# Performance work log

Hardware: AMD Instinct MI355X
Metric: run time of the kernel (lower is better)

Reference implementation:

```python
import jax, jax.numpy as jnp
import numpy as np

B, S, D, H, DH, F = 4, 2048, 1024, 16, 64, 4096
EPS = 1e-5


def setup_inputs() -> dict:
    key = jax.random.key(0)
    ks = jax.random.split(key, 8)
    std = 0.02
    return {
        "src": jax.random.normal(ks[0], (B, S, D), dtype=jnp.float32),
        # per-head Q/K/V projections, stacked: [H, D, DH]
        "Wq": jax.random.normal(ks[1], (H, D, DH), dtype=jnp.float32) * std,
        "bq": jnp.zeros((H, DH), dtype=jnp.float32),
        "Wk": jax.random.normal(ks[2], (H, D, DH), dtype=jnp.float32) * std,
        "bk": jnp.zeros((H, DH), dtype=jnp.float32),
        "Wv": jax.random.normal(ks[3], (H, D, DH), dtype=jnp.float32) * std,
        "bv": jnp.zeros((H, DH), dtype=jnp.float32),
        "Wo": jax.random.normal(ks[4], (H * DH, D), dtype=jnp.float32) * std,
        "bo": jnp.zeros((D,), dtype=jnp.float32),
        "ln1_w": jnp.ones((D,), dtype=jnp.float32),
        "ln1_b": jnp.zeros((D,), dtype=jnp.float32),
        "W1": jax.random.normal(ks[5], (D, F), dtype=jnp.float32) * std,
        "b1": jnp.zeros((F,), dtype=jnp.float32),
        "W2": jax.random.normal(ks[6], (F, D), dtype=jnp.float32) * std,
        "b2": jnp.zeros((D,), dtype=jnp.float32),
        "ln2_w": jnp.ones((D,), dtype=jnp.float32),
        "ln2_b": jnp.zeros((D,), dtype=jnp.float32),
    }


def _layernorm(x, w, b):
    m = jnp.mean(x, axis=-1, keepdims=True)
    v = jnp.mean(jnp.square(x - m), axis=-1, keepdims=True)
    return (x - m) * jax.lax.rsqrt(v + EPS) * w + b


def reference(src, Wq, bq, Wk, bk, Wv, bv, Wo, bo, ln1_w, ln1_b, W1, b1, W2, b2, ln2_w, ln2_b):
    # Per-head projections, batched over heads: [B,H,S,DH]
    q = jnp.einsum('bsd,hde->bhse', src, Wq) + bq[None, :, None, :]
    k = jnp.einsum('bsd,hde->bhse', src, Wk) + bk[None, :, None, :]
    v = jnp.einsum('bsd,hde->bhse', src, Wv) + bv[None, :, None, :]
    scale = jnp.asarray(DH, src.dtype) ** 0.5
    scores = jnp.einsum('bhqe,bhke->bhqk', q, k) / scale  # [B,H,S,S]
    attn = jax.nn.softmax(scores, axis=-1)
    ctx = jnp.einsum('bhqk,bhke->bhqe', attn, v)  # [B,H,S,DH]
    # concat heads along feature dim (matches torch.cat over head outputs)
    ctx = ctx.transpose(0, 2, 1, 3).reshape(src.shape[0], src.shape[1], H * DH)
    attn_out = ctx @ Wo + bo
    x = _layernorm(src + attn_out, ln1_w, ln1_b)
    ffn = jax.nn.relu(x @ W1 + b1) @ W2 + b2
    return _layernorm(x + ffn, ln2_w, ln2_b)
```

## Files before the change

### kernel.cpp

```cpp
#include <hip/hip_runtime.h>
#include <stdint.h>


typedef unsigned short u16;
typedef __attribute__((ext_vector_type(8))) short short8;
typedef __attribute__((ext_vector_type(4))) float f32x4;
typedef __attribute__((ext_vector_type(16))) float f32x16;

__device__ __forceinline__ u16 f2bf(float f) {
  union { float f; unsigned u; } v; v.f = f;
  unsigned r = (v.u + 0x7fffu + ((v.u >> 16) & 1u)) >> 16;
  return (u16)r;
}

__device__ __forceinline__ void gl_lds16(const u16* g, u16* l) {
  __builtin_amdgcn_global_load_lds(
      (const __attribute__((address_space(1))) unsigned int*)g,
      (__attribute__((address_space(3))) unsigned int*)l, 16, 0, 0);
}

__device__ __forceinline__ unsigned cvtpk(float lo, float hi) {
  unsigned r;
  asm("v_cvt_pk_bf16_f32 %0, %1, %2" : "=v"(r) : "v"(lo), "v"(hi));
  return r;
}
__device__ __forceinline__ void pl32_swap(unsigned& a, unsigned& b) {
  asm("v_permlane32_swap_b32 %0, %1" : "+v"(a), "+v"(b));
}


__global__ __launch_bounds__(256) void transpose_cast(const float* __restrict__ W,
                                                      u16* __restrict__ WT,
                                                      int K, int N) {
  __shared__ u16 T[64 * 72];
  const int tid = threadIdx.x;
  const long n0 = (long)blockIdx.x * 64, k0 = (long)blockIdx.y * 64;
#pragma unroll
  for (int i = 0; i < 4; i++) {
    int c = tid + i * 256;
    int kr = c >> 4, nc = (c & 15) * 4;
    float4 v = *(const float4*)(W + (k0 + kr) * N + n0 + nc);
    T[(nc + 0) * 72 + kr] = f2bf(v.x);
    T[(nc + 1) * 72 + kr] = f2bf(v.y);
    T[(nc + 2) * 72 + kr] = f2bf(v.z);
    T[(nc + 3) * 72 + kr] = f2bf(v.w);
  }
  __syncthreads();
#pragma unroll
  for (int i = 0; i < 2; i++) {
    int c = tid + i * 256;
    int nr = c >> 3, kc = (c & 7) * 8;
    *(uint4*)(WT + (n0 + nr) * K + k0 + kc) = *(const uint4*)(T + nr * 72 + kc);
  }
}

__global__ __launch_bounds__(256) void transpose_cast_qkv(const float* __restrict__ Wq,
                                                          const float* __restrict__ Wk,
                                                          const float* __restrict__ Wv,
                                                          u16* __restrict__ WT) {
  __shared__ u16 T[64 * 72];
  const int tid = threadIdx.x;
  const int n0 = blockIdx.x * 64, k0 = blockIdx.y * 64;
  const float* W = (n0 < 1024) ? Wq : (n0 < 2048 ? Wk : Wv);
  const int h = (n0 & 1023) >> 6;
#pragma unroll
  for (int i = 0; i < 4; i++) {
    int c = tid + i * 256;
    int kr = c >> 4, ec = (c & 15) * 4;
    float4 v = *(const float4*)(W + ((long)h * 1024 + k0 + kr) * 64 + ec);
    T[(ec + 0) * 72 + kr] = f2bf(v.x);
    T[(ec + 1) * 72 + kr] = f2bf(v.y);
    T[(ec + 2) * 72 + kr] = f2bf(v.z);
    T[(ec + 3) * 72 + kr] = f2bf(v.w);
  }
  __syncthreads();
#pragma unroll
  for (int i = 0; i < 2; i++) {
    int c = tid + i * 256;
    int nr = c >> 3, kc = (c & 7) * 8;
    *(uint4*)(WT + ((long)(n0 + nr)) * 1024 + k0 + kc) = *(const uint4*)(T + nr * 72 + kc);
  }
}

__global__ __launch_bounds__(256) void cast_bf16(const float* __restrict__ x, u16* __restrict__ y) {
  const long i = ((long)blockIdx.x * 256 + threadIdx.x) * 8;
  float4 a = *(const float4*)(x + i);
  float4 b = *(const float4*)(x + i + 4);
  uint4 o;
  o.x = (unsigned)f2bf(a.x) | ((unsigned)f2bf(a.y) << 16);
  o.y = (unsigned)f2bf(a.z) | ((unsigned)f2bf(a.w) << 16);
  o.z = (unsigned)f2bf(b.x) | ((unsigned)f2bf(b.y) << 16);
  o.w = (unsigned)f2bf(b.z) | ((unsigned)f2bf(b.w) << 16);
  *(uint4*)(y + i) = o;
}

__global__ __launch_bounds__(256) void build_bcat(const float* __restrict__ bq,
                                                  const float* __restrict__ bk,
                                                  const float* __restrict__ bv,
                                                  float* __restrict__ bcat) {
  int i = blockIdx.x * 256 + threadIdx.x;
  const float* s = (i < 1024) ? bq : (i < 2048 ? bk : bv);
  bcat[i] = s[i & 1023];
}

#define GEMM_PROLOGUE                                                              \
  __shared__ __align__(16) u16 As[2][128 * 32];                                    \
  __shared__ __align__(16) u16 Bs[2][128 * 32];                                    \
  const int tid = threadIdx.x;                                                     \
  const int wave = tid >> 6, lane = tid & 63, quad = lane >> 4, l15 = lane & 15;   \
  const int wm = (wave >> 1) * 64, wn = (wave & 1) * 64;                           \
  const int id = blockIdx.x, xcd = id & 7, ii = id >> 3;                           \
  const long m0 = (long)(xcd * 8 + (ii & 7)) * 128, n0 = (long)(ii >> 3) * 128;    \
  const u16* Ag = A + (m0 + (tid >> 2)) * K + (tid & 3) * 8;                       \
  const u16* Bg = B + (n0 + (tid >> 2)) * K + (tid & 3) * 8;                       \
  f32x4 acc[4][4] = {};                                                            \
  {                                                                                \
    gl_lds16(Ag, &As[0][tid * 8]);                                                 \
    gl_lds16(Ag + (long)64 * K, &As[0][tid * 8 + 2048]);                           \
    gl_lds16(Bg, &Bs[0][tid * 8]);                                                 \
    gl_lds16(Bg + (long)64 * K, &Bs[0][tid * 8 + 2048]);                           \
  }                                                                                \
  for (int k0 = 0; k0 < K; k0 += 32) {                                             \
    __syncthreads();         \
    const int cur = (k0 >> 5) & 1;                                                 \
    if (k0 + 32 < K) {                                                             \
      gl_lds16(Ag + k0 + 32, &As[cur ^ 1][tid * 8]);                               \
      gl_lds16(Ag + (long)64 * K + k0 + 32, &As[cur ^ 1][tid * 8 + 2048]);         \
      gl_lds16(Bg + k0 + 32, &Bs[cur ^ 1][tid * 8]);                               \
      gl_lds16(Bg + (long)64 * K + k0 + 32, &Bs[cur ^ 1][tid * 8 + 2048]);         \
    }                                                                              \
    short8 af[4], bfr[4];                                                          \
    _Pragma("unroll") for (int t = 0; t < 4; t++)                                  \
        af[t] = *(const short8*)(&As[cur][(wm + t * 16 + l15) * 32 + quad * 8]);   \
    _Pragma("unroll") for (int t = 0; t < 4; t++)                                  \
        bfr[t] = *(const short8*)(&Bs[cur][(wn + t * 16 + l15) * 32 + quad * 8]);  \
    _Pragma("unroll") for (int i = 0; i < 4; i++)                                  \
        _Pragma("unroll") for (int j = 0; j < 4; j++)                              \
            acc[i][j] = __builtin_amdgcn_mfma_f32_16x16x32_bf16(af[i], bfr[j],     \
                                                                acc[i][j], 0, 0, 0); \
  }

template <int MODE>
__global__ __launch_bounds__(256) void gemm_bt(const u16* __restrict__ A, const u16* __restrict__ B,
                                               const float* __restrict__ bias, void* __restrict__ Cout,
                                               int K, int N) {
  GEMM_PROLOGUE
#pragma unroll
  for (int i = 0; i < 4; i++) {
#pragma unroll
    for (int j = 0; j < 4; j++) {
      const long col = n0 + wn + j * 16 + l15;
      const float bb = bias[col];
      const long rowb = m0 + wm + i * 16 + quad * 4;
#pragma unroll
      for (int r = 0; r < 4; r++) {
        float v = acc[i][j][r] + bb;
        if (MODE == 2) v = fmaxf(v, 0.f);
        if (MODE == 0)
          ((float*)Cout)[(rowb + r) * N + col] = v;
        else
          ((u16*)Cout)[(rowb + r) * N + col] = f2bf(v);
      }
    }
  }
}

__global__ __launch_bounds__(256) void gemm_qkv(const u16* __restrict__ A, const u16* __restrict__ B,
                                                const float* __restrict__ bias,
                                                u16* __restrict__ QKb, u16* __restrict__ Vt, int K) {
  GEMM_PROLOGUE
#pragma unroll
  for (int i = 0; i < 4; i++) {
#pragma unroll
    for (int j = 0; j < 4; j++) {
      const int col0 = (int)n0 + wn + j * 16;
      const int col = col0 + l15;
      const float bb = bias[col];
      const long rowb = m0 + wm + i * 16 + quad * 4;
      if (col0 < 1024) {
#pragma unroll
        for (int r = 0; r < 4; r++)
          QKb[(rowb + r) * 2048 + col] = f2bf((acc[i][j][r] + bb) * 0.1803368801f);
      } else if (col0 < 2048) {
#pragma unroll
        for (int r = 0; r < 4; r++)
          QKb[(rowb + r) * 2048 + col] = f2bf(acc[i][j][r] + bb);
      } else {
        const int ec = col - 2048;
        const int bq = (int)(rowb >> 11), s = (int)(rowb & 2047);
        uint2 p;
        p.x = (unsigned)f2bf(acc[i][j][0] + bb) | ((unsigned)f2bf(acc[i][j][1] + bb) << 16);
        p.y = (unsigned)f2bf(acc[i][j][2] + bb) | ((unsigned)f2bf(acc[i][j][3] + bb) << 16);
        *(uint2*)(Vt + ((long)(bq * 16 + (ec >> 6)) * 64 + (ec & 63)) * 2048 + s) = p;
      }
    }
  }
}


__device__ __forceinline__ void stage_tile(const u16* __restrict__ g, u16* __restrict__ lds, int tid) {
#pragma unroll
  for (int i = 0; i < 2; i++) {
    const int s = i * 256 + tid;
    const int r = s >> 3, cs = s & 7;
    const int c = cs ^ (r & 7);
    gl_lds16(g + (long)r * 2048 + c * 8, lds + s * 8);
  }
}
__device__ __forceinline__ short8 frag(const u16* __restrict__ buf, int row, int chunk) {
  const int slot = row * 8 + (chunk ^ (row & 7));
  return *(const short8*)(buf + slot * 8);
}

__global__ __launch_bounds__(256, 2) void flash_attn(const u16* __restrict__ QKb,
                                                     const u16* __restrict__ Vt,
                                                     u16* __restrict__ ctx) {
  __shared__ __align__(16) u16 Kbuf[2][4096];
  __shared__ __align__(16) u16 Vbuf[2][4096];
  const int tid = threadIdx.x, wave = tid >> 6, lane = tid & 63;
  const int l31 = lane & 31, hi = lane >> 5;
  const int bh = blockIdx.x, b = bh >> 4, h = bh & 15;
  const int qt = blockIdx.y;
  const long qbase = (long)b * 2048 + qt * 256 + wave * 64;
  const u16* Qg = QKb + qbase * 2048 + h * 64;
  const u16* Kg = QKb + ((long)b * 2048) * 2048 + 1024 + h * 64;
  const u16* Vg = Vt + (long)bh * 64 * 2048;

  short8 qf[2][4];
#pragma unroll
  for (int j = 0; j < 2; j++)
#pragma unroll
    for (int ks = 0; ks < 4; ks++)
      qf[j][ks] = *(const short8*)(Qg + (long)(j * 32 + l31) * 2048 + ks * 16 + hi * 8);

  f32x16 O[2][2] = {};
  float rs[2] = {0.f, 0.f};

  stage_tile(Kg, Kbuf[0], tid);
  stage_tile(Vg, Vbuf[0], tid);

  for (int kt = 0; kt < 32; kt++) {
    __syncthreads();
    if (kt < 31) {
      stage_tile(Kg + (long)(kt + 1) * 64 * 2048, Kbuf[(kt + 1) & 1], tid);
      stage_tile(Vg + (kt + 1) * 64, Vbuf[(kt + 1) & 1], tid);
    }
    const u16* Kb = Kbuf[kt & 1];
    const u16* Vb = Vbuf[kt & 1];

#pragma unroll
    for (int m = 0; m < 2; m++) {
      short8 ak[4];
#pragma unroll
      for (int ks = 0; ks < 4; ks++) ak[ks] = frag(Kb, m * 32 + l31, ks * 2 + hi);
      f32x16 S[2] = {};
#pragma unroll
      for (int ks = 0; ks < 4; ks++)
#pragma unroll
        for (int j = 0; j < 2; j++)
          S[j] = __builtin_amdgcn_mfma_f32_32x32x16_bf16(ak[ks], qf[j][ks], S[j], 0, 0, 0);

      short8 pf[2][2];
#pragma unroll
      for (int j = 0; j < 2; j++) {
#pragma unroll
        for (int r = 0; r < 16; r++) S[j][r] = __builtin_amdgcn_exp2f(S[j][r]);
        rs[j] += ((S[j][0] + S[j][1]) + (S[j][2] + S[j][3])) +
                 ((S[j][4] + S[j][5]) + (S[j][6] + S[j][7])) +
                 ((S[j][8] + S[j][9]) + (S[j][10] + S[j][11])) +
                 ((S[j][12] + S[j][13]) + (S[j][14] + S[j][15]));
        unsigned w0 = cvtpk(S[j][0], S[j][1]), w1 = cvtpk(S[j][2], S[j][3]);
        unsigned w2 = cvtpk(S[j][4], S[j][5]), w3 = cvtpk(S[j][6], S[j][7]);
        unsigned w4 = cvtpk(S[j][8], S[j][9]), w5 = cvtpk(S[j][10], S[j][11]);
        unsigned w6 = cvtpk(S[j][12], S[j][13]), w7 = cvtpk(S[j][14], S[j][15]);
        pl32_swap(w2, w0); pl32_swap(w3, w1);
        pl32_swap(w6, w4); pl32_swap(w7, w5);
        union { unsigned u[4]; short8 s8; } f0, f1;
        f0.u[0] = w0; f0.u[1] = w1; f0.u[2] = w2; f0.u[3] = w3;
        f1.u[0] = w4; f1.u[1] = w5; f1.u[2] = w6; f1.u[3] = w7;
        pf[j][0] = f0.s8; pf[j][1] = f1.s8;
      }

#pragma unroll
      for (int et = 0; et < 2; et++) {
        short8 av[2];
#pragma unroll
        for (int ks2 = 0; ks2 < 2; ks2++)
          av[ks2] = frag(Vb, et * 32 + l31, m * 4 + ks2 * 2 + hi);
#pragma unroll
        for (int j = 0; j < 2; j++)
#pragma unroll
          for (int ks2 = 0; ks2 < 2; ks2++)
            O[et][j] = __builtin_amdgcn_mfma_f32_32x32x16_bf16(av[ks2], pf[j][ks2],
                                                               O[et][j], 0, 0, 0);
      }
    }
  }

#pragma unroll
  for (int j = 0; j < 2; j++) rs[j] += __shfl_xor(rs[j], 32);
#pragma unroll
  for (int j = 0; j < 2; j++) {
    const float inv = 1.f / rs[j];
    const long row = qbase + j * 32 + l31;
#pragma unroll
    for (int et = 0; et < 2; et++)
#pragma unroll
      for (int g = 0; g < 4; g++) {
        const int e0 = et * 32 + g * 8 + hi * 4;
        uint2 p;
        p.x = (unsigned)f2bf(O[et][j][g * 4 + 0] * inv) |
              ((unsigned)f2bf(O[et][j][g * 4 + 1] * inv) << 16);
        p.y = (unsigned)f2bf(O[et][j][g * 4 + 2] * inv) |
              ((unsigned)f2bf(O[et][j][g * 4 + 3] * inv) << 16);
        *(uint2*)(ctx + row * 1024 + h * 64 + e0) = p;
      }
  }
}

template <bool WB>
__global__ __launch_bounds__(256) void add_ln(const float* __restrict__ a, const float* __restrict__ c,
                                              const float* __restrict__ w, const float* __restrict__ bias,
                                              float* __restrict__ xout, u16* __restrict__ xbf) {
  const int row = blockIdx.x, tid = threadIdx.x;
  const long off = (long)row * 1024 + tid * 4;
  float4 va = *(const float4*)(a + off);
  float4 vc = *(const float4*)(c + off);
  float4 s = {va.x + vc.x, va.y + vc.y, va.z + vc.z, va.w + vc.w};
  float sum = s.x + s.y + s.z + s.w;
  float sq = s.x * s.x + s.y * s.y + s.z * s.z + s.w * s.w;
#pragma unroll
  for (int o = 32; o > 0; o >>= 1) {
    sum += __shfl_xor(sum, o);
    sq += __shfl_xor(sq, o);
  }
  __shared__ float red[8];
  const int wave = tid >> 6;
  if ((tid & 63) == 0) { red[wave] = sum; red[wave + 4] = sq; }
  __syncthreads();
  sum = red[0] + red[1] + red[2] + red[3];
  sq = red[4] + red[5] + red[6] + red[7];
  const float mean = sum * (1.f / 1024.f);
  const float var = sq * (1.f / 1024.f) - mean * mean;
  const float rstd = rsqrtf(var + 1e-5f);
  float4 vw = *(const float4*)(w + tid * 4);
  float4 vb = *(const float4*)(bias + tid * 4);
  float4 y;
  y.x = (s.x - mean) * rstd * vw.x + vb.x;
  y.y = (s.y - mean) * rstd * vw.y + vb.y;
  y.z = (s.z - mean) * rstd * vw.z + vb.z;
  y.w = (s.w - mean) * rstd * vw.w + vb.w;
  *(float4*)(xout + off) = y;
  if (WB) {
    uint2 o2;
    o2.x = (unsigned)f2bf(y.x) | ((unsigned)f2bf(y.y) << 16);
    o2.y = (unsigned)f2bf(y.z) | ((unsigned)f2bf(y.w) << 16);
    *(uint2*)(xbf + off) = o2;
  }
}

extern "C" void kernel_launch(void* const* d_in, const int* in_sizes, int n_in,
                              void* d_out, int out_size, void* d_ws, size_t ws_size,
                              hipStream_t stream) {
  (void)in_sizes; (void)n_in; (void)out_size; (void)ws_size;
  const float* src = (const float*)d_in[0];
  const float* Wq = (const float*)d_in[1];
  const float* bq = (const float*)d_in[2];
  const float* Wk = (const float*)d_in[3];
  const float* bk = (const float*)d_in[4];
  const float* Wv = (const float*)d_in[5];
  const float* bv = (const float*)d_in[6];
  const float* Wo = (const float*)d_in[7];
  const float* bo = (const float*)d_in[8];
  const float* ln1w = (const float*)d_in[9];
  const float* ln1b = (const float*)d_in[10];
  const float* W1 = (const float*)d_in[11];
  const float* b1 = (const float*)d_in[12];
  const float* W2 = (const float*)d_in[13];
  const float* b2 = (const float*)d_in[14];
  const float* ln2w = (const float*)d_in[15];
  const float* ln2b = (const float*)d_in[16];

  char* ws = (char*)d_ws;
  u16* WqkvT = (u16*)(ws + 0);
  u16* WoT = (u16*)(ws + (6ul << 20));
  u16* W1T = (u16*)(ws + (8ul << 20));
  u16* W2T = (u16*)(ws + (16ul << 20));
  float* bcat = (float*)(ws + (24ul << 20));
  u16* srcb = (u16*)(ws + (25ul << 20));
  u16* QKb = (u16*)(ws + (41ul << 20));
  u16* Vt = (u16*)(ws + (73ul << 20));
  u16* ctxb = (u16*)(ws + (89ul << 20));
  float* x = (float*)(ws + (105ul << 20));
  u16* xb = (u16*)(ws + (137ul << 20));
  u16* hb = (u16*)(ws + (41ul << 20));
  float* out = (float*)d_out;

  transpose_cast_qkv<<<dim3(48, 16), 256, 0, stream>>>(Wq, Wk, Wv, WqkvT);
  transpose_cast<<<dim3(16, 16), 256, 0, stream>>>(Wo, WoT, 1024, 1024);
  transpose_cast<<<dim3(64, 16), 256, 0, stream>>>(W1, W1T, 1024, 4096);
  transpose_cast<<<dim3(16, 64), 256, 0, stream>>>(W2, W2T, 4096, 1024);
  cast_bf16<<<4096, 256, 0, stream>>>(src, srcb);
  build_bcat<<<12, 256, 0, stream>>>(bq, bk, bv, bcat);

  gemm_qkv<<<24 * 64, 256, 0, stream>>>(srcb, WqkvT, bcat, QKb, Vt, 1024);
  flash_attn<<<dim3(64, 8), 256, 0, stream>>>(QKb, Vt, ctxb);
  gemm_bt<0><<<8 * 64, 256, 0, stream>>>(ctxb, WoT, bo, out, 1024, 1024);
  add_ln<true><<<8192, 256, 0, stream>>>(src, out, ln1w, ln1b, x, xb);
  gemm_bt<2><<<32 * 64, 256, 0, stream>>>(xb, W1T, b1, hb, 1024, 4096);
  gemm_bt<0><<<8 * 64, 256, 0, stream>>>(hb, W2T, b2, out, 4096, 1024);
  add_ln<false><<<8192, 256, 0, stream>>>(x, out, ln2w, ln2b, out, nullptr);
}
```

Baseline: 514.3 us.

## Deepen GEMM LDS pipeline to four stages with vmcnt waits and swizzle

The GEMM main loop moves from a double buffer with a full __syncthreads each step to a four-slot LDS ring that keeps three tiles in flight. It waits on explicit vmcnt counts, so the loop only blocks on the oldest outstanding load. An XOR swizzle on the 16-byte chunk index is added to reduce LDS bank conflicts on fragment reads, and bias loads are hoisted before the K loop. This doubles LDS use per block, which may lower occupancy. The hand-written waitcnt logic also assumes the compiler emits no other vector-memory ops inside the loop.

```diff
diff --git a/kernel.cpp b/kernel.cpp
--- a/kernel.cpp
+++ b/kernel.cpp
@@ -103,37 +103,46 @@
   bcat[i] = s[i & 1023];
 }
 
-#define GEMM_PROLOGUE                                                              \
-  __shared__ __align__(16) u16 As[2][128 * 32];                                    \
-  __shared__ __align__(16) u16 Bs[2][128 * 32];                                    \
+#define GEMM_SETUP                                                                 \
+  __shared__ __align__(16) u16 As[4][4096];                                        \
+  __shared__ __align__(16) u16 Bs[4][4096];                                        \
   const int tid = threadIdx.x;                                                     \
   const int wave = tid >> 6, lane = tid & 63, quad = lane >> 4, l15 = lane & 15;   \
   const int wm = (wave >> 1) * 64, wn = (wave & 1) * 64;                           \
   const int id = blockIdx.x, xcd = id & 7, ii = id >> 3;                           \
   const long m0 = (long)(xcd * 8 + (ii & 7)) * 128, n0 = (long)(ii >> 3) * 128;    \
-  const u16* Ag = A + (m0 + (tid >> 2)) * K + (tid & 3) * 8;                       \
-  const u16* Bg = B + (n0 + (tid >> 2)) * K + (tid & 3) * 8;                       \
+  const int srow = tid >> 2, sc = (tid & 3) ^ (srow & 3);                          \
+  const u16* Ag = A + (m0 + srow) * K + sc * 8;                                    \
+  const u16* Bg = B + (n0 + srow) * K + sc * 8;                                    \
+  const int cx = quad ^ (l15 & 3);                                                 \
   f32x4 acc[4][4] = {};                                                            \
-  {                                                                                \
-    gl_lds16(Ag, &As[0][tid * 8]);                                                 \
-    gl_lds16(Ag + (long)64 * K, &As[0][tid * 8 + 2048]);                           \
-    gl_lds16(Bg, &Bs[0][tid * 8]);                                                 \
-    gl_lds16(Bg + (long)64 * K, &Bs[0][tid * 8 + 2048]);                           \
-  }                                                                                \
+  _Pragma("unroll") for (int p = 0; p < 3; p++) {                                  \
+    gl_lds16(Ag + p * 32, &As[p][tid * 8]);                                        \
+    gl_lds16(Ag + (long)64 * K + p * 32, &As[p][tid * 8 + 2048]);                  \
+    gl_lds16(Bg + p * 32, &Bs[p][tid * 8]);                                        \
+    gl_lds16(Bg + (long)64 * K + p * 32, &Bs[p][tid * 8 + 2048]);                  \
+  }
+
+#define GEMM_KLOOP                                                                 \
   for (int k0 = 0; k0 < K; k0 += 32) {                                             \
-    __syncthreads();         \
-    const int cur = (k0 >> 5) & 1;                                                 \
-    if (k0 + 32 < K) {                                                             \
-      gl_lds16(Ag + k0 + 32, &As[cur ^ 1][tid * 8]);                               \
-      gl_lds16(Ag + (long)64 * K + k0 + 32, &As[cur ^ 1][tid * 8 + 2048]);         \
-      gl_lds16(Bg + k0 + 32, &Bs[cur ^ 1][tid * 8]);                               \
-      gl_lds16(Bg + (long)64 * K + k0 + 32, &Bs[cur ^ 1][tid * 8 + 2048]);         \
+    if (K - k0 >= 96) asm volatile("s_waitcnt vmcnt(8)" ::: "memory");             \
+    else if (K - k0 == 64) asm volatile("s_waitcnt vmcnt(4)" ::: "memory");        \
+    else asm volatile("s_waitcnt vmcnt(0)" ::: "memory");                          \
+    __builtin_amdgcn_s_barrier();                                                  \
+    __builtin_amdgcn_sched_barrier(0);                                             \
+    const int cur = (k0 >> 5) & 3;                                                 \
+    if (k0 + 96 < K) {                                                             \
+      const int nb = (cur + 3) & 3;                                                \
+      gl_lds16(Ag + k0 + 96, &As[nb][tid * 8]);                                    \
+      gl_lds16(Ag + (long)64 * K + k0 + 96, &As[nb][tid * 8 + 2048]);              \
+      gl_lds16(Bg + k0 + 96, &Bs[nb][tid * 8]);                                    \
+      gl_lds16(Bg + (long)64 * K + k0 + 96, &Bs[nb][tid * 8 + 2048]);              \
     }                                                                              \
     short8 af[4], bfr[4];                                                          \
     _Pragma("unroll") for (int t = 0; t < 4; t++)                                  \
-        af[t] = *(const short8*)(&As[cur][(wm + t * 16 + l15) * 32 + quad * 8]);   \
+        af[t] = *(const short8*)(&As[cur][(wm + t * 16 + l15) * 32 + cx * 8]);     \
     _Pragma("unroll") for (int t = 0; t < 4; t++)                                  \
-        bfr[t] = *(const short8*)(&Bs[cur][(wn + t * 16 + l15) * 32 + quad * 8]);  \
+        bfr[t] = *(const short8*)(&Bs[cur][(wn + t * 16 + l15) * 32 + cx * 8]);    \
     _Pragma("unroll") for (int i = 0; i < 4; i++)                                  \
         _Pragma("unroll") for (int j = 0; j < 4; j++)                              \
             acc[i][j] = __builtin_amdgcn_mfma_f32_16x16x32_bf16(af[i], bfr[j],     \
@@ -144,17 +153,20 @@
 __global__ __launch_bounds__(256) void gemm_bt(const u16* __restrict__ A, const u16* __restrict__ B,
                                                const float* __restrict__ bias, void* __restrict__ Cout,
                                                int K, int N) {
-  GEMM_PROLOGUE
+  GEMM_SETUP
+  float bb[4];
+#pragma unroll
+  for (int j = 0; j < 4; j++) bb[j] = bias[n0 + wn + j * 16 + l15];
+  GEMM_KLOOP
 #pragma unroll
   for (int i = 0; i < 4; i++) {
 #pragma unroll
     for (int j = 0; j < 4; j++) {
       const long col = n0 + wn + j * 16 + l15;
-      const float bb = bias[col];
       const long rowb = m0 + wm + i * 16 + quad * 4;
 #pragma unroll
       for (int r = 0; r < 4; r++) {
-        float v = acc[i][j][r] + bb;
+        float v = acc[i][j][r] + bb[j];
         if (MODE == 2) v = fmaxf(v, 0.f);
         if (MODE == 0)
           ((float*)Cout)[(rowb + r) * N + col] = v;
@@ -168,29 +180,32 @@
 __global__ __launch_bounds__(256) void gemm_qkv(const u16* __restrict__ A, const u16* __restrict__ B,
                                                 const float* __restrict__ bias,
                                                 u16* __restrict__ QKb, u16* __restrict__ Vt, int K) {
-  GEMM_PROLOGUE
+  GEMM_SETUP
+  float bb[4];
+#pragma unroll
+  for (int j = 0; j < 4; j++) bb[j] = bias[n0 + wn + j * 16 + l15];
+  GEMM_KLOOP
 #pragma unroll
   for (int i = 0; i < 4; i++) {
 #pragma unroll
     for (int j = 0; j < 4; j++) {
       const int col0 = (int)n0 + wn + j * 16;
       const int col = col0 + l15;
-      const float bb = bias[col];
       const long rowb = m0 + wm + i * 16 + quad * 4;
       if (col0 < 1024) {
 #pragma unroll
         for (int r = 0; r < 4; r++)
-          QKb[(rowb + r) * 2048 + col] = f2bf((acc[i][j][r] + bb) * 0.1803368801f);
+          QKb[(rowb + r) * 2048 + col] = f2bf((acc[i][j][r] + bb[j]) * 0.1803368801f);
       } else if (col0 < 2048) {
 #pragma unroll
         for (int r = 0; r < 4; r++)
-          QKb[(rowb + r) * 2048 + col] = f2bf(acc[i][j][r] + bb);
+          QKb[(rowb + r) * 2048 + col] = f2bf(acc[i][j][r] + bb[j]);
       } else {
         const int ec = col - 2048;
         const int bq = (int)(rowb >> 11), s = (int)(rowb & 2047);
         uint2 p;
-        p.x = (unsigned)f2bf(acc[i][j][0] + bb) | ((unsigned)f2bf(acc[i][j][1] + bb) << 16);
-        p.y = (unsigned)f2bf(acc[i][j][2] + bb) | ((unsigned)f2bf(acc[i][j][3] + bb) << 16);
+        p.x = (unsigned)f2bf(acc[i][j][0] + bb[j]) | ((unsigned)f2bf(acc[i][j][1] + bb[j]) << 16);
+        p.y = (unsigned)f2bf(acc[i][j][2] + bb[j]) | ((unsigned)f2bf(acc[i][j][3] + bb[j]) << 16);
         *(uint2*)(Vt + ((long)(bq * 16 + (ec >> 6)) * 64 + (ec & 63)) * 2048 + s) = p;
       }
     }
```

New measurement: 555.0 us. 7.9% more time.

## Swizzle GEMM LDS layout and split-K the N=1024 GEMMs within a block

Applied to the files above, without the earlier changes.

The shared GEMM prologue now XOR-swizzles the 16-byte column chunk per row when staging A/B tiles into LDS, and the fragment reads undo the swizzle. This is meant to cut LDS bank conflicts on the short8 reads. A new 512-thread kernel splits K across two groups of four waves for the output projection and the second FFN GEMM, then reduces the partial sums through LDS before the epilogue. Those two GEMMs launch only 512 blocks, so the split is meant to raise wave occupancy per CU, at the cost of doubled LDS use and an extra reduction pass.

```diff
diff --git a/kernel.cpp b/kernel.cpp
--- a/kernel.cpp
+++ b/kernel.cpp
@@ -104,22 +104,22 @@
 }
 
 #define GEMM_PROLOGUE                                                              \
-  __shared__ __align__(16) u16 As[2][128 * 32];                                    \
-  __shared__ __align__(16) u16 Bs[2][128 * 32];                                    \
+  __shared__ __align__(16) u16 As[2][4096];                                        \
+  __shared__ __align__(16) u16 Bs[2][4096];                                        \
   const int tid = threadIdx.x;                                                     \
   const int wave = tid >> 6, lane = tid & 63, quad = lane >> 4, l15 = lane & 15;   \
   const int wm = (wave >> 1) * 64, wn = (wave & 1) * 64;                           \
   const int id = blockIdx.x, xcd = id & 7, ii = id >> 3;                           \
   const long m0 = (long)(xcd * 8 + (ii & 7)) * 128, n0 = (long)(ii >> 3) * 128;    \
-  const u16* Ag = A + (m0 + (tid >> 2)) * K + (tid & 3) * 8;                       \
-  const u16* Bg = B + (n0 + (tid >> 2)) * K + (tid & 3) * 8;                       \
+  const int srow = tid >> 2, sc = (tid & 3) ^ ((srow >> 1) & 3);                   \
+  const u16* Ag = A + (m0 + srow) * K + sc * 8;                                    \
+  const u16* Bg = B + (n0 + srow) * K + sc * 8;                                    \
+  const int cx = (l15 >> 1) & 3;                                                   \
   f32x4 acc[4][4] = {};                                                            \
-  {                                                                                \
-    gl_lds16(Ag, &As[0][tid * 8]);                                                 \
-    gl_lds16(Ag + (long)64 * K, &As[0][tid * 8 + 2048]);                           \
-    gl_lds16(Bg, &Bs[0][tid * 8]);                                                 \
-    gl_lds16(Bg + (long)64 * K, &Bs[0][tid * 8 + 2048]);                           \
-  }                                                                                \
+  gl_lds16(Ag, &As[0][tid * 8]);                                                   \
+  gl_lds16(Ag + (long)64 * K, &As[0][tid * 8 + 2048]);                             \
+  gl_lds16(Bg, &Bs[0][tid * 8]);                                                   \
+  gl_lds16(Bg + (long)64 * K, &Bs[0][tid * 8 + 2048]);                             \
   for (int k0 = 0; k0 < K; k0 += 32) {                                             \
     __syncthreads();         \
     const int cur = (k0 >> 5) & 1;                                                 \
@@ -131,9 +131,9 @@
     }                                                                              \
     short8 af[4], bfr[4];                                                          \
     _Pragma("unroll") for (int t = 0; t < 4; t++)                                  \
-        af[t] = *(const short8*)(&As[cur][(wm + t * 16 + l15) * 32 + quad * 8]);   \
+        af[t] = *(const short8*)(&As[cur][(wm + t * 16 + l15) * 32 + (quad ^ cx) * 8]); \
     _Pragma("unroll") for (int t = 0; t < 4; t++)                                  \
-        bfr[t] = *(const short8*)(&Bs[cur][(wn + t * 16 + l15) * 32 + quad * 8]);  \
+        bfr[t] = *(const short8*)(&Bs[cur][(wn + t * 16 + l15) * 32 + (quad ^ cx) * 8]); \
     _Pragma("unroll") for (int i = 0; i < 4; i++)                                  \
         _Pragma("unroll") for (int j = 0; j < 4; j++)                              \
             acc[i][j] = __builtin_amdgcn_mfma_f32_16x16x32_bf16(af[i], bfr[j],     \
@@ -160,6 +160,85 @@
           ((float*)Cout)[(rowb + r) * N + col] = v;
         else
           ((u16*)Cout)[(rowb + r) * N + col] = f2bf(v);
+      }
+    }
+  }
+}
+
+template <int MODE>
+__global__ __launch_bounds__(512) void gemm_bt_sk(const u16* __restrict__ A, const u16* __restrict__ B,
+                                                  const float* __restrict__ bias, void* __restrict__ Cout,
+                                                  int K, int N) {
+  __shared__ __align__(16) u16 As[2][2][4096];
+  __shared__ __align__(16) u16 Bs[2][2][4096];
+  const int tid = threadIdx.x;
+  const int wave = tid >> 6, lane = tid & 63, quad = lane >> 4, l15 = lane & 15;
+  const int kh = wave >> 2, w4 = wave & 3;
+  const int wm = (w4 >> 1) * 64, wn = (w4 & 1) * 64;
+  const int id = blockIdx.x, xcd = id & 7, ii = id >> 3;
+  const long m0 = (long)(xcd * 8 + (ii & 7)) * 128, n0 = (long)(ii >> 3) * 128;
+  const int t = tid & 255;
+  const int srow = t >> 2, sc = (t & 3) ^ ((srow >> 1) & 3);
+  const int Kh = K >> 1;
+  const u16* Ag = A + (m0 + srow) * K + kh * Kh + sc * 8;
+  const u16* Bg = B + (n0 + srow) * K + kh * Kh + sc * 8;
+  const int cx = (l15 >> 1) & 3;
+  f32x4 acc[4][4] = {};
+  gl_lds16(Ag, &As[kh][0][t * 8]);
+  gl_lds16(Ag + (long)64 * K, &As[kh][0][t * 8 + 2048]);
+  gl_lds16(Bg, &Bs[kh][0][t * 8]);
+  gl_lds16(Bg + (long)64 * K, &Bs[kh][0][t * 8 + 2048]);
+  for (int k0 = 0; k0 < Kh; k0 += 32) {
+    __syncthreads();
+    const int cur = (k0 >> 5) & 1;
+    if (k0 + 32 < Kh) {
+      gl_lds16(Ag + k0 + 32, &As[kh][cur ^ 1][t * 8]);
+      gl_lds16(Ag + (long)64 * K + k0 + 32, &As[kh][cur ^ 1][t * 8 + 2048]);
+      gl_lds16(Bg + k0 + 32, &Bs[kh][cur ^ 1][t * 8]);
+      gl_lds16(Bg + (long)64 * K + k0 + 32, &Bs[kh][cur ^ 1][t * 8 + 2048]);
+    }
+    short8 af[4], bfr[4];
+#pragma unroll
+    for (int tt = 0; tt < 4; tt++)
+      af[tt] = *(const short8*)(&As[kh][cur][(wm + tt * 16 + l15) * 32 + (quad ^ cx) * 8]);
+#pragma unroll
+    for (int tt = 0; tt < 4; tt++)
+      bfr[tt] = *(const short8*)(&Bs[kh][cur][(wn + tt * 16 + l15) * 32 + (quad ^ cx) * 8]);
+#pragma unroll
+    for (int i = 0; i < 4; i++)
+#pragma unroll
+      for (int j = 0; j < 4; j++)
+        acc[i][j] = __builtin_amdgcn_mfma_f32_16x16x32_bf16(af[i], bfr[j], acc[i][j], 0, 0, 0);
+  }
+  __syncthreads();
+  float* red = (w4 & 2) ? (float*)Bs : (float*)As;
+  float* myred = red + (w4 & 1) * 4096 + lane * 4;
+  if (kh == 1) {
+#pragma unroll
+    for (int i = 0; i < 4; i++)
+#pragma unroll
+      for (int j = 0; j < 4; j++)
+        *(f32x4*)(myred + (i * 4 + j) * 256) = acc[i][j];
+  }
+  __syncthreads();
+  if (kh == 0) {
+#pragma unroll
+    for (int i = 0; i < 4; i++) {
+#pragma unroll
+      for (int j = 0; j < 4; j++) {
+        const f32x4 o = *(const f32x4*)(myred + (i * 4 + j) * 256);
+        const long col = n0 + wn + j * 16 + l15;
+        const float bb = bias[col];
+        const long rowb = m0 + wm + i * 16 + quad * 4;
+#pragma unroll
+        for (int r = 0; r < 4; r++) {
+          float v = acc[i][j][r] + o[r] + bb;
+          if (MODE == 2) v = fmaxf(v, 0.f);
+          if (MODE == 0)
+            ((float*)Cout)[(rowb + r) * N + col] = v;
+          else
+            ((u16*)Cout)[(rowb + r) * N + col] = f2bf(v);
+        }
       }
     }
   }
@@ -405,9 +484,9 @@
 
   gemm_qkv<<<24 * 64, 256, 0, stream>>>(srcb, WqkvT, bcat, QKb, Vt, 1024);
   flash_attn<<<dim3(64, 8), 256, 0, stream>>>(QKb, Vt, ctxb);
-  gemm_bt<0><<<8 * 64, 256, 0, stream>>>(ctxb, WoT, bo, out, 1024, 1024);
+  gemm_bt_sk<0><<<8 * 64, 512, 0, stream>>>(ctxb, WoT, bo, out, 1024, 1024);
   add_ln<true><<<8192, 256, 0, stream>>>(src, out, ln1w, ln1b, x, xb);
   gemm_bt<2><<<32 * 64, 256, 0, stream>>>(xb, W1T, b1, hb, 1024, 4096);
-  gemm_bt<0><<<8 * 64, 256, 0, stream>>>(hb, W2T, b2, out, 4096, 1024);
+  gemm_bt_sk<0><<<8 * 64, 512, 0, stream>>>(hb, W2T, b2, out, 4096, 1024);
   add_ln<false><<<8192, 256, 0, stream>>>(x, out, ln2w, ln2b, out, nullptr);
 }
```

Measured after the change: 511.6 us, median of 2. No clear change (-0.5%).

## Split K across two wave groups in GEMMs with LDS reduction and swizzle

Applied to the files above, without the earlier changes.

All GEMM kernels now launch 512 threads per block. The two halves of the block each process half of the K dimension with their own double-buffered LDS tiles, and the partial accumulators are reduced through shared memory before the epilogue. The LDS layout also gains an XOR swizzle on the chunk index to reduce bank conflicts on fragment reads. This doubles the waves available per tile to hide latency, at the cost of an extra LDS reduction pass, twice the shared memory per block, and possibly lower block occupancy.

```diff
diff --git a/kernel.cpp b/kernel.cpp
--- a/kernel.cpp
+++ b/kernel.cpp
@@ -103,95 +103,117 @@
   bcat[i] = s[i & 1023];
 }
 
-#define GEMM_PROLOGUE                                                              \
-  __shared__ __align__(16) u16 As[2][128 * 32];                                    \
-  __shared__ __align__(16) u16 Bs[2][128 * 32];                                    \
+#define GEMM_SK_CORE                                                               \
+  __shared__ __align__(16) u16 As[2][2][4096];                      \
+  __shared__ __align__(16) u16 Bs[2][2][4096];                                     \
   const int tid = threadIdx.x;                                                     \
   const int wave = tid >> 6, lane = tid & 63, quad = lane >> 4, l15 = lane & 15;   \
-  const int wm = (wave >> 1) * 64, wn = (wave & 1) * 64;                           \
+  const int kh = wave >> 2, w4 = wave & 3;                                         \
+  const int wm = (w4 >> 1) * 64, wn = (w4 & 1) * 64;                               \
   const int id = blockIdx.x, xcd = id & 7, ii = id >> 3;                           \
   const long m0 = (long)(xcd * 8 + (ii & 7)) * 128, n0 = (long)(ii >> 3) * 128;    \
-  const u16* Ag = A + (m0 + (tid >> 2)) * K + (tid & 3) * 8;                       \
-  const u16* Bg = B + (n0 + (tid >> 2)) * K + (tid & 3) * 8;                       \
+  const int t = tid & 255;                         \
+  const int srow = t >> 2, sc = (t & 3) ^ ((srow >> 1) & 3);                       \
+  const int Kh = K >> 1;                                                           \
+  const u16* Ag = A + (m0 + srow) * K + kh * Kh + sc * 8;                          \
+  const u16* Bg = B + (n0 + srow) * K + kh * Kh + sc * 8;                          \
+  const int cx = (l15 >> 1) & 3;                                                   \
   f32x4 acc[4][4] = {};                                                            \
-  {                                                                                \
-    gl_lds16(Ag, &As[0][tid * 8]);                                                 \
-    gl_lds16(Ag + (long)64 * K, &As[0][tid * 8 + 2048]);                           \
-    gl_lds16(Bg, &Bs[0][tid * 8]);                                                 \
-    gl_lds16(Bg + (long)64 * K, &Bs[0][tid * 8 + 2048]);                           \
-  }                                                                                \
-  for (int k0 = 0; k0 < K; k0 += 32) {                                             \
-    __syncthreads();         \
+  gl_lds16(Ag, &As[kh][0][t * 8]);                                                 \
+  gl_lds16(Ag + (long)64 * K, &As[kh][0][t * 8 + 2048]);                           \
+  gl_lds16(Bg, &Bs[kh][0][t * 8]);                                                 \
+  gl_lds16(Bg + (long)64 * K, &Bs[kh][0][t * 8 + 2048]);                           \
+  for (int k0 = 0; k0 < Kh; k0 += 32) {                                            \
+    __syncthreads();                                                               \
     const int cur = (k0 >> 5) & 1;                                                 \
-    if (k0 + 32 < K) {                                                             \
-      gl_lds16(Ag + k0 + 32, &As[cur ^ 1][tid * 8]);                               \
-      gl_lds16(Ag + (long)64 * K + k0 + 32, &As[cur ^ 1][tid * 8 + 2048]);         \
-      gl_lds16(Bg + k0 + 32, &Bs[cur ^ 1][tid * 8]);                               \
-      gl_lds16(Bg + (long)64 * K + k0 + 32, &Bs[cur ^ 1][tid * 8 + 2048]);         \
+    if (k0 + 32 < Kh) {                                                            \
+      gl_lds16(Ag + k0 + 32, &As[kh][cur ^ 1][t * 8]);                             \
+      gl_lds16(Ag + (long)64 * K + k0 + 32, &As[kh][cur ^ 1][t * 8 + 2048]);       \
+      gl_lds16(Bg + k0 + 32, &Bs[kh][cur ^ 1][t * 8]);                             \
+      gl_lds16(Bg + (long)64 * K + k0 + 32, &Bs[kh][cur ^ 1][t * 8 + 2048]);       \
     }                                                                              \
     short8 af[4], bfr[4];                                                          \
-    _Pragma("unroll") for (int t = 0; t < 4; t++)                                  \
-        af[t] = *(const short8*)(&As[cur][(wm + t * 16 + l15) * 32 + quad * 8]);   \
-    _Pragma("unroll") for (int t = 0; t < 4; t++)                                  \
-        bfr[t] = *(const short8*)(&Bs[cur][(wn + t * 16 + l15) * 32 + quad * 8]);  \
+    _Pragma("unroll") for (int tt = 0; tt < 4; tt++)                               \
+        af[tt] = *(const short8*)(&As[kh][cur][(wm + tt * 16 + l15) * 32 + (quad ^ cx) * 8]); \
+    _Pragma("unroll") for (int tt = 0; tt < 4; tt++)                               \
+        bfr[tt] = *(const short8*)(&Bs[kh][cur][(wn + tt * 16 + l15) * 32 + (quad ^ cx) * 8]); \
     _Pragma("unroll") for (int i = 0; i < 4; i++)                                  \
         _Pragma("unroll") for (int j = 0; j < 4; j++)                              \
             acc[i][j] = __builtin_amdgcn_mfma_f32_16x16x32_bf16(af[i], bfr[j],     \
                                                                 acc[i][j], 0, 0, 0); \
-  }
+  }                                                                                \
+                  \
+  __syncthreads();                                                                 \
+  float* red = (w4 & 2) ? (float*)Bs : (float*)As;                                 \
+  float* myred = red + (w4 & 1) * 4096 + lane * 4;                                 \
+  if (kh == 1) {                                                                   \
+    _Pragma("unroll") for (int i = 0; i < 4; i++)                                  \
+        _Pragma("unroll") for (int j = 0; j < 4; j++)                              \
+            *(f32x4*)(myred + (i * 4 + j) * 256) = acc[i][j];                      \
+  }                                                                                \
+  __syncthreads();
 
 template <int MODE>
-__global__ __launch_bounds__(256) void gemm_bt(const u16* __restrict__ A, const u16* __restrict__ B,
-                                               const float* __restrict__ bias, void* __restrict__ Cout,
-                                               int K, int N) {
-  GEMM_PROLOGUE
-#pragma unroll
-  for (int i = 0; i < 4; i++) {
-#pragma unroll
-    for (int j = 0; j < 4; j++) {
-      const long col = n0 + wn + j * 16 + l15;
-      const float bb = bias[col];
-      const long rowb = m0 + wm + i * 16 + quad * 4;
-#pragma unroll
-      for (int r = 0; r < 4; r++) {
-        float v = acc[i][j][r] + bb;
-        if (MODE == 2) v = fmaxf(v, 0.f);
-        if (MODE == 0)
-          ((float*)Cout)[(rowb + r) * N + col] = v;
-        else
-          ((u16*)Cout)[(rowb + r) * N + col] = f2bf(v);
+__global__ __launch_bounds__(512) void gemm_bt_sk(const u16* __restrict__ A, const u16* __restrict__ B,
+                                                  const float* __restrict__ bias, void* __restrict__ Cout,
+                                                  int K, int N) {
+  GEMM_SK_CORE
+  if (kh == 0) {
+#pragma unroll
+    for (int i = 0; i < 4; i++) {
+#pragma unroll
+      for (int j = 0; j < 4; j++) {
+        const f32x4 o = *(const f32x4*)(myred + (i * 4 + j) * 256);
+        const long col = n0 + wn + j * 16 + l15;
+        const float bb = bias[col];
+        const long rowb = m0 + wm + i * 16 + quad * 4;
+#pragma unroll
+        for (int r = 0; r < 4; r++) {
+          float v = acc[i][j][r] + o[r] + bb;
+          if (MODE == 2) v = fmaxf(v, 0.f);
+          if (MODE == 0)
+            ((float*)Cout)[(rowb + r) * N + col] = v;
+          else
+            ((u16*)Cout)[(rowb + r) * N + col] = f2bf(v);
+        }
       }
     }
   }
 }
 
-__global__ __launch_bounds__(256) void gemm_qkv(const u16* __restrict__ A, const u16* __restrict__ B,
-                                                const float* __restrict__ bias,
-                                                u16* __restrict__ QKb, u16* __restrict__ Vt, int K) {
-  GEMM_PROLOGUE
-#pragma unroll
-  for (int i = 0; i < 4; i++) {
-#pragma unroll
-    for (int j = 0; j < 4; j++) {
-      const int col0 = (int)n0 + wn + j * 16;
-      const int col = col0 + l15;
-      const float bb = bias[col];
-      const long rowb = m0 + wm + i * 16 + quad * 4;
-      if (col0 < 1024) {
-#pragma unroll
-        for (int r = 0; r < 4; r++)
-          QKb[(rowb + r) * 2048 + col] = f2bf((acc[i][j][r] + bb) * 0.1803368801f);
-      } else if (col0 < 2048) {
-#pragma unroll
-        for (int r = 0; r < 4; r++)
-          QKb[(rowb + r) * 2048 + col] = f2bf(acc[i][j][r] + bb);
-      } else {
-        const int ec = col - 2048;
-        const int bq = (int)(rowb >> 11), s = (int)(rowb & 2047);
-        uint2 p;
-        p.x = (unsigned)f2bf(acc[i][j][0] + bb) | ((unsigned)f2bf(acc[i][j][1] + bb) << 16);
-        p.y = (unsigned)f2bf(acc[i][j][2] + bb) | ((unsigned)f2bf(acc[i][j][3] + bb) << 16);
-        *(uint2*)(Vt + ((long)(bq * 16 + (ec >> 6)) * 64 + (ec & 63)) * 2048 + s) = p;
+__global__ __launch_bounds__(512) void gemm_qkv_sk(const u16* __restrict__ A, const u16* __restrict__ B,
+                                                   const float* __restrict__ bias,
+                                                   u16* __restrict__ QKb, u16* __restrict__ Vt, int K) {
+  GEMM_SK_CORE
+  if (kh == 0) {
+#pragma unroll
+    for (int i = 0; i < 4; i++) {
+#pragma unroll
+      for (int j = 0; j < 4; j++) {
+        const f32x4 o = *(const f32x4*)(myred + (i * 4 + j) * 256);
+        const int col0 = (int)n0 + wn + j * 16;
+        const int col = col0 + l15;
+        const float bb = bias[col];
+        const long rowb = m0 + wm + i * 16 + quad * 4;
+        float v[4];
+#pragma unroll
+        for (int r = 0; r < 4; r++) v[r] = acc[i][j][r] + o[r] + bb;
+        if (col0 < 1024) {
+#pragma unroll
+          for (int r = 0; r < 4; r++)
+            QKb[(rowb + r) * 2048 + col] = f2bf(v[r] * 0.1803368801f);
+        } else if (col0 < 2048) {
+#pragma unroll
+          for (int r = 0; r < 4; r++)
+            QKb[(rowb + r) * 2048 + col] = f2bf(v[r]);
+        } else {
+          const int ec = col - 2048;
+          const int bq = (int)(rowb >> 11), s = (int)(rowb & 2047);
+          uint2 p;
+          p.x = (unsigned)f2bf(v[0]) | ((unsigned)f2bf(v[1]) << 16);
+          p.y = (unsigned)f2bf(v[2]) | ((unsigned)f2bf(v[3]) << 16);
+          *(uint2*)(Vt + ((long)(bq * 16 + (ec >> 6)) * 64 + (ec & 63)) * 2048 + s) = p;
+        }
       }
     }
   }
@@ -403,11 +425,11 @@
   cast_bf16<<<4096, 256, 0, stream>>>(src, srcb);
   build_bcat<<<12, 256, 0, stream>>>(bq, bk, bv, bcat);
 
-  gemm_qkv<<<24 * 64, 256, 0, stream>>>(srcb, WqkvT, bcat, QKb, Vt, 1024);
+  gemm_qkv_sk<<<24 * 64, 512, 0, stream>>>(srcb, WqkvT, bcat, QKb, Vt, 1024);
   flash_attn<<<dim3(64, 8), 256, 0, stream>>>(QKb, Vt, ctxb);
-  gemm_bt<0><<<8 * 64, 256, 0, stream>>>(ctxb, WoT, bo, out, 1024, 1024);
+  gemm_bt_sk<0><<<8 * 64, 512, 0, stream>>>(ctxb, WoT, bo, out, 1024, 1024);
   add_ln<true><<<8192, 256, 0, stream>>>(src, out, ln1w, ln1b, x, xb);
-  gemm_bt<2><<<32 * 64, 256, 0, stream>>>(xb, W1T, b1, hb, 1024, 4096);
-  gemm_bt<0><<<8 * 64, 256, 0, stream>>>(hb, W2T, b2, out, 4096, 1024);
+  gemm_bt_sk<2><<<32 * 64, 512, 0, stream>>>(xb, W1T, b1, hb, 1024, 4096);
+  gemm_bt_sk<0><<<8 * 64, 512, 0, stream>>>(hb, W2T, b2, out, 4096, 1024);
   add_ln<false><<<8192, 256, 0, stream>>>(x, out, ln2w, ln2b, out, nullptr);
 }
```

New measurement: 535.5 us. 4.1% more time.
